# Optimization experiments

Measured on AMD Instinct MI355X. Metric: run time of the kernel, lower is better.

## Reference

```python
import jax, jax.numpy as jnp
import numpy as np
import math

C, H, L, V = 1024, 16, 2, 32000
D = C // H  # head_dim = 64
FF = 4 * C
B, T = 1, 2048
EPS = 1e-5

def _alibi_slopes(n_heads):
    start = 2 ** (-2 ** (-(math.log2(n_heads) - 3)))
    return np.array([start * start ** i for i in range(n_heads)], dtype=np.float32)

SLOPES = jnp.asarray(_alibi_slopes(H))

def _sym_ln(x, w, b):
    # per-head-channel LayerNorm over head_dim, scalar scale/bias per head
    xh = x.reshape(x.shape[0], x.shape[1], H, D)
    mu = xh.mean(-1, keepdims=True)
    var = ((xh - mu) ** 2).mean(-1, keepdims=True)
    n = (xh - mu) / jnp.sqrt(var + EPS)
    n = n * w[None, None, :, None] + b[None, None, :, None]
    return n.reshape(x.shape)

def _alibi_bias(t):
    pos = jnp.arange(t)[None, :] - jnp.arange(t)[:, None]  # j - i
    pos = jnp.minimum(pos, 0).astype(jnp.float32)
    return SLOPES[:, None, None] * pos[None, :, :]  # (H, T, T)

def _block(x, ln1_w, ln1_b, ln2_w, ln2_b, attn_w, attn_b, v_tmp, proj_tmp, fc_w, fc_b, pw, pb):
    b_, t_, _ = x.shape
    h_in = _sym_ln(x, ln1_w, ln1_b)
    qk = h_in @ attn_w.T + attn_b  # (B, T, 2C)
    q, k = jnp.split(qk, 2, axis=-1)
    # Kronecker/block-diagonal V: per-head (head_dim x head_dim) matmul, x @ M^T per head
    xh = h_in.reshape(b_, t_, H, D)
    v = jnp.einsum('bthd,hed->bthe', xh, v_tmp)  # (B, T, H, D)
    q = q.reshape(b_, t_, H, D).transpose(0, 2, 1, 3)
    k = k.reshape(b_, t_, H, D).transpose(0, 2, 1, 3)
    v = v.transpose(0, 2, 1, 3)
    scale = 1.0 / math.sqrt(D)
    scores = jnp.einsum('bhqd,bhkd->bhqk', q, k) * scale
    scores = scores + _alibi_bias(t_)[None]  # note: no causal mask in original code
    att = jax.nn.softmax(scores, axis=-1)
    y = jnp.einsum('bhqk,bhkd->bhqd', att, v)
    y = y.transpose(0, 2, 1, 3)  # (B, T, H, D)
    y = jnp.einsum('bthd,hed->bthe', y, proj_tmp).reshape(b_, t_, C)
    x = x + y
    h2 = _sym_ln(x, ln2_w, ln2_b)
    f = jax.nn.gelu(h2 @ fc_w.T + fc_b, approximate=False)
    x = x + (f @ pw.T + pb)
    return x

def setup_inputs() -> dict:
    key = jax.random.key(0)
    ks = jax.random.split(key, 12)
    s = 0.02
    return {
        'idx': jax.random.randint(ks[0], (B, T), 0, V, dtype=jnp.int32),
        'wte': jax.random.normal(ks[1], (V, C), jnp.float32) * s,
        'ln1_w': jnp.ones((L, H), jnp.float32),
        'ln1_b': jnp.zeros((L, H), jnp.float32),
        'ln2_w': jnp.ones((L, H), jnp.float32),
        'ln2_b': jnp.zeros((L, H), jnp.float32),
        'lnf_w': jnp.ones((H,), jnp.float32),
        'lnf_b': jnp.zeros((H,), jnp.float32),
        'attn_w': jax.random.normal(ks[2], (L, 2 * C, C), jnp.float32) * s,
        'attn_b': jnp.zeros((L, 2 * C), jnp.float32),
        'v_tmp': jax.random.normal(ks[3], (L, H, D, D), jnp.float32) * s,
        'proj_tmp': jax.random.normal(ks[4], (L, H, D, D), jnp.float32) * s,
        'fc_w': jax.random.normal(ks[5], (L, FF, C), jnp.float32) * s,
        'fc_b': jnp.zeros((L, FF), jnp.float32),
        'proj_w': jax.random.normal(ks[6], (L, C, FF), jnp.float32) * s,
        'proj_b': jnp.zeros((L, C), jnp.float32),
    }

def reference(idx, wte, ln1_w, ln1_b, ln2_w, ln2_b, lnf_w, lnf_b,
              attn_w, attn_b, v_tmp, proj_tmp, fc_w, fc_b, proj_w, proj_b):
    x = wte[idx]  # (B, T, C)
    for l in range(L):
        x = _block(x, ln1_w[l], ln1_b[l], ln2_w[l], ln2_b[l],
                   attn_w[l], attn_b[l], v_tmp[l], proj_tmp[l],
                   fc_w[l], fc_b[l], proj_w[l], proj_b[l])
    x = _sym_ln(x, lnf_w, lnf_b)
    logits = x @ wte.T  # tied lm_head
    return logits
```

## Files before the change

### kernel.cpp

```cpp
#include <hip/hip_runtime.h>
#include <cstdint>
#include <cstddef>

#define T_SEQ 2048
#define C_DIM 1024
#define H_HEADS 16
#define D_HEAD 64
#define FF_DIM 4096
#define V_VOCAB 32000
#define L_LAYERS 2

typedef unsigned short u16;
typedef short bf16x8 __attribute__((ext_vector_type(8)));
typedef float f32x4 __attribute__((ext_vector_type(4)));

__device__ inline u16 f2bf(float f) {
  unsigned u = __float_as_uint(f);
  u += 0x7fffu + ((u >> 16) & 1u);
  return (u16)(u >> 16);
}
__device__ inline float bf2f(u16 h) { return __uint_as_float(((unsigned)h) << 16); }

#define OFF_WTEBF   0ULL
#define OFF_ATTNBF  65536000ULL
#define OFF_FCBF    73924608ULL
#define OFF_PRJBF   90701824ULL
#define OFF_X       107479040ULL
#define OFF_HBF     115867648ULL
#define OFF_QKBF    120061952ULL
#define OFF_VT      128450560ULL
#define OFF_Y       132644864ULL
#define OFF_FBF     141033472ULL
#define OFF_VWBF    157810688ULL
#define OFF_PWBF    158072832ULL
#define ARENA_BYTES 158334976ULL

__device__ __align__(1024) unsigned char g_arena[ARENA_BYTES];

__global__ void cvt_bf16_k(const float4* __restrict__ in, ushort4* __restrict__ out, int n4) {
  int i = blockIdx.x * 256 + threadIdx.x;
  if (i < n4) {
    float4 v = in[i];
    out[i] = make_ushort4(f2bf(v.x), f2bf(v.y), f2bf(v.z), f2bf(v.w));
  }
}

__global__ void cvt_multi_k(const float4* __restrict__ s0, const float4* __restrict__ s1,
                            const float4* __restrict__ s2, const float4* __restrict__ s3,
                            const float4* __restrict__ s4,
                            ushort4* __restrict__ d0, ushort4* __restrict__ d1,
                            ushort4* __restrict__ d2, ushort4* __restrict__ d3,
                            ushort4* __restrict__ d4) {
  int g = blockIdx.x * 256 + threadIdx.x;
  const float4* s; ushort4* d; int off;
  if (g < 1048576)      { s = s0; d = d0; off = g; }
  else if (g < 3145728) { s = s1; d = d1; off = g - 1048576; }
  else if (g < 5242880) { s = s2; d = d2; off = g - 3145728; }
  else if (g < 5275648) { s = s3; d = d3; off = g - 5242880; }
  else                  { s = s4; d = d4; off = g - 5275648; }
  float4 v = s[off];
  d[off] = make_ushort4(f2bf(v.x), f2bf(v.y), f2bf(v.z), f2bf(v.w));
}

__global__ void embed_k(const int* __restrict__ idx, const float4* __restrict__ wte,
                        float4* __restrict__ x) {
  int t = blockIdx.x;
  int r = idx[t];
  x[(size_t)t * 256 + threadIdx.x] = wte[(size_t)r * 256 + threadIdx.x];
}

__global__ void symln_k(const float* __restrict__ x, const float* __restrict__ w,
                        const float* __restrict__ b, u16* __restrict__ out) {
  int t = blockIdx.x;
  int wv = threadIdx.x >> 6, lane = threadIdx.x & 63;
  #pragma unroll
  for (int hh = 0; hh < 4; hh++) {
    int h = wv * 4 + hh;
    float v = x[(size_t)t * C_DIM + h * 64 + lane];
    float s = v, s2 = v * v;
    #pragma unroll
    for (int m = 32; m; m >>= 1) { s += __shfl_xor(s, m); s2 += __shfl_xor(s2, m); }
    float mu = s * (1.f / 64.f);
    float var = s2 * (1.f / 64.f) - mu * mu;
    float n = (v - mu) * rsqrtf(var + 1e-5f) * w[h] + b[h];
    out[(size_t)t * C_DIM + h * 64 + lane] = f2bf(n);
  }
}

template <int NROWS, int ROWBYTES, int WAVES>
__device__ inline void stage_rows(u16* lds, const u16* __restrict__ g, int ld,
                                  int wid, int lane) {
  constexpr int PASSES = (NROWS * ROWBYTES) / (WAVES * 1024);
  #pragma unroll
  for (int i = 0; i < PASSES; i++) {
    int base = (i * WAVES + wid) * 1024;
    int o = base + lane * 16;
    int u = o ^ (((o / ROWBYTES) & 7) << 4);
    int row = u / ROWBYTES, colb = u % ROWBYTES;
    const u16* src = g + (size_t)row * ld + (colb >> 1);
    __builtin_amdgcn_global_load_lds((const __attribute__((address_space(1))) void*)src,
                                     (__attribute__((address_space(3))) void*)(lds + base / 2),
                                     16, 0, 0);
  }
}

__device__ inline void stage_pass(u16* lds, const u16* __restrict__ g, int ld,
                                  int i, int wid, int lane) {
  int base = (i * 8 + wid) * 1024;
  int o = base + lane * 16;
  int u = o ^ (((o >> 7) & 7) << 4);
  int row = u >> 7, colb = u & 127;
  const u16* src = g + (size_t)row * ld + (colb >> 1);
  __builtin_amdgcn_global_load_lds((const __attribute__((address_space(1))) void*)src,
                                   (__attribute__((address_space(3))) void*)(lds + base / 2),
                                   16, 0, 0);
}

__global__ __launch_bounds__(256) void flash_k(const u16* __restrict__ qk,
                                               const u16* __restrict__ vt,
                                               u16* __restrict__ y) {
  int h = blockIdx.y;
  int q0 = blockIdx.x * 64;
  int tid = threadIdx.x, wid = tid >> 6, lane = tid & 63;
  int g4 = lane >> 4, l15 = lane & 15;
  __shared__ u16 Kl[128 * 64];
  __shared__ u16 Vl[64 * 128];
  __shared__ u16 Pl[64 * 128];
  float slope = exp2f(-0.5f * (float)(h + 1));

  bf16x8 qf[2];
  const u16* qb = qk + (size_t)(q0 + wid * 16) * 2048 + h * 64;
  #pragma unroll
  for (int kk = 0; kk < 2; kk++)
    qf[kk] = *(const bf16x8*)(qb + (size_t)l15 * 2048 + kk * 32 + g4 * 8);

  f32x4 lsum = (f32x4){0.f, 0.f, 0.f, 0.f};
  f32x4 oacc[4];
  #pragma unroll
  for (int n = 0; n < 4; n++) oacc[n] = (f32x4){0.f, 0.f, 0.f, 0.f};

  const u16* kbase = qk + 1024 + h * 64;
  const u16* vbase = vt + (size_t)h * 64 * T_SEQ;

  for (int kt = 0; kt < T_SEQ / 128; kt++) {
    int k0 = kt * 128;
    stage_rows<128, 128, 4>(Kl, kbase + (size_t)k0 * 2048, 2048, wid, lane);
    stage_rows<64, 256, 4>(Vl, vbase + k0, T_SEQ, wid, lane);
    __syncthreads();

    f32x4 s[8];
    #pragma unroll
    for (int n = 0; n < 8; n++) s[n] = (f32x4){0.f, 0.f, 0.f, 0.f};
    #pragma unroll
    for (int kk = 0; kk < 2; kk++) {
      #pragma unroll
      for (int n = 0; n < 8; n++) {
        int r = n * 16 + l15;
        int b = (r * 128 + kk * 64 + g4 * 16) ^ ((r & 7) << 4);
        bf16x8 kf = *(const bf16x8*)((const char*)Kl + b);
        s[n] = __builtin_amdgcn_mfma_f32_16x16x32_bf16(qf[kk], kf, s[n], 0, 0, 0);
      }
    }

    int iq = q0 + wid * 16 + g4 * 4;
    #pragma unroll
    for (int n = 0; n < 8; n++) {
      int j = k0 + n * 16 + l15;
      #pragma unroll
      for (int i = 0; i < 4; i++) {
        float v = s[n][i] * 0.125f + slope * fminf((float)(j - (iq + i)), 0.f);
        float p = __expf(v - 8.f);
        lsum[i] += p;
        int pr = wid * 16 + g4 * 4 + i;
        int b = (pr * 256 + (n * 16 + l15) * 2) ^ ((pr & 7) << 4);
        *(u16*)((char*)Pl + b) = f2bf(p);
      }
    }

    #pragma unroll
    for (int kk = 0; kk < 4; kk++) {
      int pr = wid * 16 + l15;
      int pb = (pr * 256 + kk * 64 + g4 * 16) ^ ((pr & 7) << 4);
      bf16x8 pa = *(const bf16x8*)((const char*)Pl + pb);
      #pragma unroll
      for (int n = 0; n < 4; n++) {
        int d = n * 16 + l15;
        int vb = (d * 256 + kk * 64 + g4 * 16) ^ ((d & 7) << 4);
        bf16x8 vf = *(const bf16x8*)((const char*)Vl + vb);
        oacc[n] = __builtin_amdgcn_mfma_f32_16x16x32_bf16(pa, vf, oacc[n], 0, 0, 0);
      }
    }
    __syncthreads();
  }

  #pragma unroll
  for (int i = 0; i < 4; i++) {
    float v = lsum[i];
    #pragma unroll
    for (int msk = 1; msk <= 8; msk <<= 1) v += __shfl_xor(v, msk);
    lsum[i] = v;
  }
  u16* yb = y + (size_t)(q0 + wid * 16) * C_DIM + h * 64;
  #pragma unroll
  for (int n = 0; n < 4; n++)
    #pragma unroll
    for (int i = 0; i < 4; i++)
      yb[(size_t)(g4 * 4 + i) * C_DIM + n * 16 + l15] = f2bf(oacc[n][i] / lsum[i]);
}

#define ASM_VMCNT0 asm volatile("s_waitcnt vmcnt(0)" ::: "memory")

__global__ __launch_bounds__(512, 1) void gemm256_k(const u16* __restrict__ A, int lda,
                                                    const u16* __restrict__ B, int ldb,
                                                    float* __restrict__ C, int ldc,
                                                    int K, int MT) {
  extern __shared__ u16 sm[];
  u16* lsA = sm;
  u16* lsB = sm + 32768;
  int tid = threadIdx.x, wid = tid >> 6, lane = tid & 63;
  int g4 = lane >> 4, l15 = lane & 15;
  int wm = wid >> 2, wn = wid & 3;
  int nwg = gridDim.x, lin = blockIdx.x;
  int chunk = nwg >> 3;
  int w = (lin & 7) * chunk + (lin >> 3);
  int by = w % MT, bx = w / MT;
  const u16* Ab = A + (size_t)(by * 256) * lda;
  const u16* Bb = B + (size_t)(bx * 256) * ldb;

  f32x4 acc[8][4];
  #pragma unroll
  for (int m = 0; m < 8; m++)
    #pragma unroll
    for (int n = 0; n < 4; n++) acc[m][n] = (f32x4){0.f, 0.f, 0.f, 0.f};

  int NT = K >> 6;
  stage_rows<256, 128, 8>(lsA, Ab, lda, wid, lane);
  stage_rows<256, 128, 8>(lsB, Bb, ldb, wid, lane);

  for (int t = 0; t < NT; ++t) {
    int cur = t & 1;
    const char* cA = (const char*)(lsA + cur * 16384);
    const char* cB = (const char*)(lsB + cur * 16384);
    u16* nAl = lsA + (cur ^ 1) * 16384;
    u16* nBl = lsB + (cur ^ 1) * 16384;
    const u16* gA = Ab + (t + 1) * 64;
    const u16* gB = Bb + (t + 1) * 64;
    bool pf = (t + 1 < NT);

    ASM_VMCNT0;
    __builtin_amdgcn_s_barrier();
    __builtin_amdgcn_sched_barrier(0);

    bf16x8 bfr[4], af[4];
    #pragma unroll
    for (int ph = 0; ph < 4; ++ph) {
      const int kk = ph >> 1, mh = ph & 1;
      if (mh == 0) {
        #pragma unroll
        for (int n = 0; n < 4; n++) {
          int r = wn * 64 + n * 16 + l15;
          bfr[n] = *(const bf16x8*)(cB + ((r * 128 + kk * 64 + g4 * 16) ^ ((r & 7) << 4)));
        }
      }
      #pragma unroll
      for (int m = 0; m < 4; m++) {
        int r = wm * 128 + mh * 64 + m * 16 + l15;
        af[m] = *(const bf16x8*)(cA + ((r * 128 + kk * 64 + g4 * 16) ^ ((r & 7) << 4)));
      }
      if (pf) {
        if (ph == 0) { stage_pass(nAl, gA, lda, 0, wid, lane);
                       stage_pass(nAl, gA, lda, 1, wid, lane);
                       stage_pass(nBl, gB, ldb, 0, wid, lane); }
        else if (ph == 1) { stage_pass(nAl, gA, lda, 2, wid, lane);
                            stage_pass(nAl, gA, lda, 3, wid, lane);
                            stage_pass(nBl, gB, ldb, 1, wid, lane); }
        else if (ph == 2) { stage_pass(nBl, gB, ldb, 2, wid, lane);
                            stage_pass(nBl, gB, ldb, 3, wid, lane); }
      }
      __builtin_amdgcn_s_setprio(1);
      #pragma unroll
      for (int m = 0; m < 4; m++)
        #pragma unroll
        for (int n = 0; n < 4; n++)
          acc[mh * 4 + m][n] =
              __builtin_amdgcn_mfma_f32_16x16x32_bf16(af[m], bfr[n], acc[mh * 4 + m][n], 0, 0, 0);
      __builtin_amdgcn_s_setprio(0);
      __builtin_amdgcn_s_barrier();
    }
  }

  int gr0 = by * 256 + wm * 128, gc0 = bx * 256 + wn * 64;
  #pragma unroll
  for (int m = 0; m < 8; m++)
    #pragma unroll
    for (int n = 0; n < 4; n++)
      #pragma unroll
      for (int i = 0; i < 4; i++)
        C[(size_t)(gr0 + m * 16 + g4 * 4 + i) * ldc + gc0 + n * 16 + l15] = acc[m][n][i];
}

template <int BM, int BN, int WM, int WN, int EPI, int MT, int GRID>
__global__ void gemm_nt(const u16* __restrict__ A, int lda, long long sA,
                        const u16* __restrict__ B, int ldb, long long sB,
                        void* __restrict__ C, int ldc, long long sC,
                        int K, const float* __restrict__ bias,
                        const float* __restrict__ resid, int ldr) {
  constexpr int RM = BM / WM, RN = BN / WN;
  constexpr int MR = RM / 16, NR = RN / 16;
  __shared__ u16 lsA[BM * 64];
  __shared__ u16 lsB[BN * 64];
  int tid = threadIdx.x, wid = tid >> 6, lane = tid & 63;
  int wm = wid / WN, wn = wid % WN;
  int lin, z;
  if constexpr (GRID == 1) {
    lin = blockIdx.x; z = blockIdx.y;
  } else {
    int nwg = gridDim.x, l0 = blockIdx.x;
    int chunk = nwg >> 3;
    lin = (l0 & 7) * chunk + (l0 >> 3);
    z = 0;
  }
  int by = lin % MT, bx = lin / MT;
  int row0 = by * BM, col0 = bx * BN;
  const u16* Ab = A + (size_t)z * sA + (size_t)row0 * lda;
  const u16* Bb = B + (size_t)z * sB + (size_t)col0 * ldb;
  size_t cz = (size_t)z * sC;

  f32x4 acc[MR][NR];
  #pragma unroll
  for (int m = 0; m < MR; m++)
    #pragma unroll
    for (int n = 0; n < NR; n++) acc[m][n] = (f32x4){0.f, 0.f, 0.f, 0.f};

  for (int k0 = 0; k0 < K; k0 += 64) {
    stage_rows<BM, 128, 4>(lsA, Ab + k0, lda, wid, lane);
    stage_rows<BN, 128, 4>(lsB, Bb + k0, ldb, wid, lane);
    __syncthreads();
    #pragma unroll
    for (int kk = 0; kk < 2; kk++) {
      bf16x8 af[MR], bfr[NR];
      #pragma unroll
      for (int m = 0; m < MR; m++) {
        int r = wm * RM + m * 16 + (lane & 15);
        int bofs = (r * 128 + kk * 64 + ((lane >> 4) * 16)) ^ ((r & 7) << 4);
        af[m] = *(const bf16x8*)((const char*)lsA + bofs);
      }
      #pragma unroll
      for (int n = 0; n < NR; n++) {
        int r = wn * RN + n * 16 + (lane & 15);
        int bofs = (r * 128 + kk * 64 + ((lane >> 4) * 16)) ^ ((r & 7) << 4);
        bfr[n] = *(const bf16x8*)((const char*)lsB + bofs);
      }
      #pragma unroll
      for (int m = 0; m < MR; m++)
        #pragma unroll
        for (int n = 0; n < NR; n++)
          acc[m][n] = __builtin_amdgcn_mfma_f32_16x16x32_bf16(af[m], bfr[n], acc[m][n], 0, 0, 0);
    }
    __syncthreads();
  }

  int rbase = row0 + wm * RM, cbase = col0 + wn * RN;
  #pragma unroll
  for (int m = 0; m < MR; m++)
    #pragma unroll
    for (int n = 0; n < NR; n++)
      #pragma unroll
      for (int i = 0; i < 4; i++) {
        int gr = rbase + m * 16 + ((lane >> 4) * 4) + i;
        int gc = cbase + n * 16 + (lane & 15);
        size_t idx = cz + (size_t)gr * ldc + gc;
        float v = acc[m][n][i];
        if constexpr (EPI == 0) {
          ((float*)C)[idx] = v;
        } else if constexpr (EPI == 1) {
          v += bias[gc];
          ((u16*)C)[idx] = f2bf(v);
        } else if constexpr (EPI == 2) {
          ((u16*)C)[idx] = f2bf(v);
        } else if constexpr (EPI == 3) {
          v += bias[gc];
          v = 0.5f * v * (1.f + erff(v * 0.70710678118654752f));
          ((u16*)C)[idx] = f2bf(v);
        } else if constexpr (EPI == 4) {
          v += bias[gc] + resid[(size_t)gr * ldr + gc];
          ((float*)C)[idx] = v;
        } else {
          ((float*)C)[idx] += v;
        }
      }
}

extern "C" void kernel_launch(void* const* d_in, const int* in_sizes, int n_in,
                              void* d_out, int out_size, void* d_ws, size_t ws_size,
                              hipStream_t stream) {
  (void)in_sizes; (void)n_in; (void)out_size; (void)d_ws; (void)ws_size;
  const int*   idx    = (const int*)d_in[0];
  const float* wte    = (const float*)d_in[1];
  const float* ln1w   = (const float*)d_in[2];
  const float* ln1b   = (const float*)d_in[3];
  const float* ln2w   = (const float*)d_in[4];
  const float* ln2b   = (const float*)d_in[5];
  const float* lnfw   = (const float*)d_in[6];
  const float* lnfb   = (const float*)d_in[7];
  const float* attw   = (const float*)d_in[8];
  const float* attb   = (const float*)d_in[9];
  const float* vtmp   = (const float*)d_in[10];
  const float* ptmp   = (const float*)d_in[11];
  const float* fcw    = (const float*)d_in[12];
  const float* fcb    = (const float*)d_in[13];
  const float* prjw   = (const float*)d_in[14];
  const float* prjb   = (const float*)d_in[15];
  float* out = (float*)d_out;

  unsigned char* ar = nullptr;
  hipGetSymbolAddress((void**)&ar, HIP_SYMBOL(g_arena));
  u16*   wtebf  = (u16*)(ar + OFF_WTEBF);
  u16*   attnbf = (u16*)(ar + OFF_ATTNBF);
  u16*   fcbf   = (u16*)(ar + OFF_FCBF);
  u16*   prjbf  = (u16*)(ar + OFF_PRJBF);
  float* x      = (float*)(ar + OFF_X);
  u16*   hbf    = (u16*)(ar + OFF_HBF);
  u16*   qkbf   = (u16*)(ar + OFF_QKBF);
  u16*   vt     = (u16*)(ar + OFF_VT);
  u16*   ybf    = (u16*)(ar + OFF_Y);
  u16*   fbf    = (u16*)(ar + OFF_FBF);
  u16*   vwbf   = (u16*)(ar + OFF_VWBF);
  u16*   pwbf   = (u16*)(ar + OFF_PWBF);

  hipFuncSetAttribute((const void*)gemm256_k,
                      hipFuncAttributeMaxDynamicSharedMemorySize, 131072);

  cvt_bf16_k<<<dim3((V_VOCAB * C_DIM / 4) / 256), 256, 0, stream>>>(
      (const float4*)wte, (ushort4*)wtebf, V_VOCAB * C_DIM / 4);
  cvt_multi_k<<<dim3(20736), 256, 0, stream>>>(
      (const float4*)attw, (const float4*)fcw, (const float4*)prjw,
      (const float4*)vtmp, (const float4*)ptmp,
      (ushort4*)attnbf, (ushort4*)fcbf, (ushort4*)prjbf,
      (ushort4*)vwbf, (ushort4*)pwbf);

  embed_k<<<dim3(T_SEQ), 256, 0, stream>>>(idx, (const float4*)wte, (float4*)x);

  for (int l = 0; l < L_LAYERS; l++) {
    symln_k<<<dim3(T_SEQ), 256, 0, stream>>>(x, ln1w + l * H_HEADS, ln1b + l * H_HEADS, hbf);
    gemm_nt<64, 128, 2, 2, 1, 32, 0><<<dim3((2 * C_DIM / 128) * (T_SEQ / 64)), 256, 0, stream>>>(
        hbf, C_DIM, 0, attnbf + (size_t)l * 2 * C_DIM * C_DIM, C_DIM, 0,
        qkbf, 2 * C_DIM, 0, C_DIM, attb + l * 2 * C_DIM, nullptr, 0);
    gemm_nt<64, 128, 2, 2, 2, 1, 1><<<dim3(T_SEQ / 128, H_HEADS), 256, 0, stream>>>(
        vwbf + (size_t)l * H_HEADS * 4096, 64, 4096, hbf, C_DIM, 64,
        vt, T_SEQ, (long long)64 * T_SEQ, 64, nullptr, nullptr, 0);
    flash_k<<<dim3(T_SEQ / 64, H_HEADS), 256, 0, stream>>>(qkbf, vt, ybf);
    gemm_nt<128, 64, 4, 1, 5, 16, 1><<<dim3(T_SEQ / 128, H_HEADS), 256, 0, stream>>>(
        ybf, C_DIM, 64, pwbf + (size_t)l * H_HEADS * 4096, 64, 4096,
        x, C_DIM, 64, 64, nullptr, nullptr, 0);
    symln_k<<<dim3(T_SEQ), 256, 0, stream>>>(x, ln2w + l * H_HEADS, ln2b + l * H_HEADS, hbf);
    gemm_nt<128, 128, 2, 2, 3, 16, 0><<<dim3((FF_DIM / 128) * (T_SEQ / 128)), 256, 0, stream>>>(
        hbf, C_DIM, 0, fcbf + (size_t)l * FF_DIM * C_DIM, C_DIM, 0,
        fbf, FF_DIM, 0, C_DIM, fcb + l * FF_DIM, nullptr, 0);
    gemm_nt<64, 128, 2, 2, 4, 32, 0><<<dim3((C_DIM / 128) * (T_SEQ / 64)), 256, 0, stream>>>(
        fbf, FF_DIM, 0, prjbf + (size_t)l * C_DIM * FF_DIM, FF_DIM, 0,
        x, C_DIM, 0, FF_DIM, prjb + l * C_DIM, x, C_DIM);
  }
  symln_k<<<dim3(T_SEQ), 256, 0, stream>>>(x, lnfw, lnfb, hbf);
  gemm256_k<<<dim3((V_VOCAB / 256) * (T_SEQ / 256)), 512, 131072, stream>>>(
      hbf, C_DIM, wtebf, C_DIM, out, V_VOCAB, C_DIM, T_SEQ / 256);
}
```

Before: 600.6 us.

## Double-buffer K tiles in LDS and load V straight into registers

The flash attention kernel now keeps two LDS buffers for K and prefetches the next 128-key tile while the current one is being used. V is no longer staged through LDS: each wave loads its V fragments directly from global memory into registers. This removes the trailing per-iteration __syncthreads and some of the LDS traffic, so K loads for the next tile overlap with compute. The cost is that every wave reads the full V tile, which multiplies global/L2 reads of V, and the V fragments take extra VGPRs, which may lower occupancy.

Measured after the change: 739.3 us. 1.23x slower.

```diff
diff --git a/kernel.cpp b/kernel.cpp
--- a/kernel.cpp
+++ b/kernel.cpp
@@ -123,8 +123,7 @@
   int q0 = blockIdx.x * 64;
   int tid = threadIdx.x, wid = tid >> 6, lane = tid & 63;
   int g4 = lane >> 4, l15 = lane & 15;
-  __shared__ u16 Kl[128 * 64];
-  __shared__ u16 Vl[64 * 128];
+  __shared__ u16 Kl[2][128 * 64];
   __shared__ u16 Pl[64 * 128];
   float slope = exp2f(-0.5f * (float)(h + 1));
 
@@ -142,11 +141,27 @@
   const u16* kbase = qk + 1024 + h * 64;
   const u16* vbase = vt + (size_t)h * 64 * T_SEQ;
 
+  stage_rows<128, 128, 4>(Kl[0], kbase, 2048, wid, lane);
+
   for (int kt = 0; kt < T_SEQ / 128; kt++) {
     int k0 = kt * 128;
-    stage_rows<128, 128, 4>(Kl, kbase + (size_t)k0 * 2048, 2048, wid, lane);
-    stage_rows<64, 256, 4>(Vl, vbase + k0, T_SEQ, wid, lane);
-    __syncthreads();
+    const char* cK = (const char*)Kl[kt & 1];
+    asm volatile("s_waitcnt vmcnt(0)" ::: "memory");
+    __builtin_amdgcn_s_barrier();
+    __builtin_amdgcn_sched_barrier(0);
+
+    bf16x8 vf[4][4];
+    #pragma unroll
+    for (int kk = 0; kk < 4; kk++)
+      #pragma unroll
+      for (int n = 0; n < 4; n++)
+        vf[kk][n] = *(const bf16x8*)(vbase + (size_t)(n * 16 + l15) * T_SEQ +
+                                     k0 + kk * 32 + g4 * 8);
+    __builtin_amdgcn_sched_barrier(0);
+
+    if (kt + 1 < T_SEQ / 128)
+      stage_rows<128, 128, 4>(Kl[(kt + 1) & 1], kbase + (size_t)(k0 + 128) * 2048,
+                              2048, wid, lane);
 
     f32x4 s[8];
     #pragma unroll
@@ -157,7 +172,7 @@
       for (int n = 0; n < 8; n++) {
         int r = n * 16 + l15;
         int b = (r * 128 + kk * 64 + g4 * 16) ^ ((r & 7) << 4);
-        bf16x8 kf = *(const bf16x8*)((const char*)Kl + b);
+        bf16x8 kf = *(const bf16x8*)(cK + b);
         s[n] = __builtin_amdgcn_mfma_f32_16x16x32_bf16(qf[kk], kf, s[n], 0, 0, 0);
       }
     }
@@ -183,14 +198,9 @@
       int pb = (pr * 256 + kk * 64 + g4 * 16) ^ ((pr & 7) << 4);
       bf16x8 pa = *(const bf16x8*)((const char*)Pl + pb);
       #pragma unroll
-      for (int n = 0; n < 4; n++) {
-        int d = n * 16 + l15;
-        int vb = (d * 256 + kk * 64 + g4 * 16) ^ ((d & 7) << 4);
-        bf16x8 vf = *(const bf16x8*)((const char*)Vl + vb);
-        oacc[n] = __builtin_amdgcn_mfma_f32_16x16x32_bf16(pa, vf, oacc[n], 0, 0, 0);
-      }
+      for (int n = 0; n < 4; n++)
+        oacc[n] = __builtin_amdgcn_mfma_f32_16x16x32_bf16(pa, vf[kk][n], oacc[n], 0, 0, 0);
     }
-    __syncthreads();
   }
 
   #pragma unroll
```

## Split flash attention across key dimension with separate combine kernel

Applied to the files above, without the earlier changes.

Flash attention now splits the key range into four chunks along a new grid z dimension. Each block writes unnormalized fp32 partial outputs and row sums to a scratch arena. A new combine kernel sums the partials, normalizes them and writes the bf16 output. This raises block count and occupancy for attention, at the cost of extra global traffic and one more launch per layer.

Measured after the change: 619.7 us. 3.2% more time.

```diff
diff --git a/kernel.cpp b/kernel.cpp
--- a/kernel.cpp
+++ b/kernel.cpp
@@ -9,6 +9,7 @@
 #define FF_DIM 4096
 #define V_VOCAB 32000
 #define L_LAYERS 2
+#define NSPLIT 4
 
 typedef unsigned short u16;
 typedef short bf16x8 __attribute__((ext_vector_type(8)));
@@ -33,7 +34,9 @@
 #define OFF_FBF     141033472ULL
 #define OFF_VWBF    157810688ULL
 #define OFF_PWBF    158072832ULL
-#define ARENA_BYTES 158334976ULL
+#define OFF_OPART   158334976ULL
+#define OFF_LPART   191889408ULL
+#define ARENA_BYTES 192413696ULL
 
 __device__ __align__(1024) unsigned char g_arena[ARENA_BYTES];
 
@@ -118,9 +121,11 @@
 
 __global__ __launch_bounds__(256) void flash_k(const u16* __restrict__ qk,
                                                const u16* __restrict__ vt,
-                                               u16* __restrict__ y) {
+                                               float* __restrict__ opart,
+                                               float* __restrict__ lpart) {
   int h = blockIdx.y;
   int q0 = blockIdx.x * 64;
+  int zs = blockIdx.z;
   int tid = threadIdx.x, wid = tid >> 6, lane = tid & 63;
   int g4 = lane >> 4, l15 = lane & 15;
   __shared__ u16 Kl[128 * 64];
@@ -142,7 +147,7 @@
   const u16* kbase = qk + 1024 + h * 64;
   const u16* vbase = vt + (size_t)h * 64 * T_SEQ;
 
-  for (int kt = 0; kt < T_SEQ / 128; kt++) {
+  for (int kt = zs * 4; kt < zs * 4 + 4; kt++) {
     int k0 = kt * 128;
     stage_rows<128, 128, 4>(Kl, kbase + (size_t)k0 * 2048, 2048, wid, lane);
     stage_rows<64, 256, 4>(Vl, vbase + k0, T_SEQ, wid, lane);
@@ -200,12 +205,35 @@
     for (int msk = 1; msk <= 8; msk <<= 1) v += __shfl_xor(v, msk);
     lsum[i] = v;
   }
-  u16* yb = y + (size_t)(q0 + wid * 16) * C_DIM + h * 64;
+  float* ob = opart + ((size_t)zs * T_SEQ + q0 + wid * 16) * C_DIM + h * 64;
   #pragma unroll
   for (int n = 0; n < 4; n++)
     #pragma unroll
     for (int i = 0; i < 4; i++)
-      yb[(size_t)(g4 * 4 + i) * C_DIM + n * 16 + l15] = f2bf(oacc[n][i] / lsum[i]);
+      ob[(size_t)(g4 * 4 + i) * C_DIM + n * 16 + l15] = oacc[n][i];
+  if (l15 == 0) {
+    #pragma unroll
+    for (int i = 0; i < 4; i++)
+      lpart[((size_t)zs * H_HEADS + h) * T_SEQ + q0 + wid * 16 + g4 * 4 + i] = lsum[i];
+  }
+}
+
+__global__ void fcomb_k(const float* __restrict__ opart, const float* __restrict__ lpart,
+                        u16* __restrict__ y) {
+  int t = blockIdx.x;
+  int c = threadIdx.x * 4;
+  int h = c >> 6;
+  float4 s = make_float4(0.f, 0.f, 0.f, 0.f);
+  float l = 0.f;
+  #pragma unroll
+  for (int z = 0; z < NSPLIT; z++) {
+    float4 o = *(const float4*)(opart + ((size_t)z * T_SEQ + t) * C_DIM + c);
+    s.x += o.x; s.y += o.y; s.z += o.z; s.w += o.w;
+    l += lpart[((size_t)z * H_HEADS + h) * T_SEQ + t];
+  }
+  float inv = 1.f / l;
+  *(ushort4*)(y + (size_t)t * C_DIM + c) =
+      make_ushort4(f2bf(s.x * inv), f2bf(s.y * inv), f2bf(s.z * inv), f2bf(s.w * inv));
 }
 
 #define ASM_VMCNT0 asm volatile("s_waitcnt vmcnt(0)" ::: "memory")
@@ -427,6 +455,8 @@
   u16*   fbf    = (u16*)(ar + OFF_FBF);
   u16*   vwbf   = (u16*)(ar + OFF_VWBF);
   u16*   pwbf   = (u16*)(ar + OFF_PWBF);
+  float* opart  = (float*)(ar + OFF_OPART);
+  float* lpart  = (float*)(ar + OFF_LPART);
 
   hipFuncSetAttribute((const void*)gemm256_k,
                       hipFuncAttributeMaxDynamicSharedMemorySize, 131072);
@@ -449,7 +479,8 @@
     gemm_nt<64, 128, 2, 2, 2, 1, 1><<<dim3(T_SEQ / 128, H_HEADS), 256, 0, stream>>>(
         vwbf + (size_t)l * H_HEADS * 4096, 64, 4096, hbf, C_DIM, 64,
         vt, T_SEQ, (long long)64 * T_SEQ, 64, nullptr, nullptr, 0);
-    flash_k<<<dim3(T_SEQ / 64, H_HEADS), 256, 0, stream>>>(qkbf, vt, ybf);
+    flash_k<<<dim3(T_SEQ / 64, H_HEADS, NSPLIT), 256, 0, stream>>>(qkbf, vt, opart, lpart);
+    fcomb_k<<<dim3(T_SEQ), 256, 0, stream>>>(opart, lpart, ybf);
     gemm_nt<128, 64, 4, 1, 5, 16, 1><<<dim3(T_SEQ / 128, H_HEADS), 256, 0, stream>>>(
         ybf, C_DIM, 64, pwbf + (size_t)l * H_HEADS * 4096, 64, 4096,
         x, C_DIM, 64, 64, nullptr, nullptr, 0);
```

## Transpose QK^T MFMA in flash kernel, pack P stores, retile FC GEMM

Applied to the files above, without the earlier changes.

The flash attention kernel swaps the MFMA operands so each lane holds scores for a single query row across four consecutive keys. That lets the softmax write probabilities as packed bf16x4 stores via v_cvt_pk_bf16_f32 instead of scalar u16 stores, and keeps one scalar row sum that needs only two cross-lane shuffles. The final normalisation multiplies by a reciprocal instead of dividing. Separately, the FC GEMM tile changes from 128x128 to 64x128, doubling the grid, which trades per-block reuse for more parallelism.

Result: faster. 560.2 us (-6.7%).

```diff
diff --git a/kernel.cpp b/kernel.cpp
--- a/kernel.cpp
+++ b/kernel.cpp
@@ -134,13 +134,14 @@
   for (int kk = 0; kk < 2; kk++)
     qf[kk] = *(const bf16x8*)(qb + (size_t)l15 * 2048 + kk * 32 + g4 * 8);
 
-  f32x4 lsum = (f32x4){0.f, 0.f, 0.f, 0.f};
+  float lsum = 0.f;
   f32x4 oacc[4];
   #pragma unroll
   for (int n = 0; n < 4; n++) oacc[n] = (f32x4){0.f, 0.f, 0.f, 0.f};
 
   const u16* kbase = qk + 1024 + h * 64;
   const u16* vbase = vt + (size_t)h * 64 * T_SEQ;
+  int myq = q0 + wid * 16 + l15;
 
   for (int kt = 0; kt < T_SEQ / 128; kt++) {
     int k0 = kt * 128;
@@ -158,28 +159,31 @@
         int r = n * 16 + l15;
         int b = (r * 128 + kk * 64 + g4 * 16) ^ ((r & 7) << 4);
         bf16x8 kf = *(const bf16x8*)((const char*)Kl + b);
-        s[n] = __builtin_amdgcn_mfma_f32_16x16x32_bf16(qf[kk], kf, s[n], 0, 0, 0);
+        s[n] = __builtin_amdgcn_mfma_f32_16x16x32_bf16(kf, qf[kk], s[n], 0, 0, 0);
       }
     }
 
-    int iq = q0 + wid * 16 + g4 * 4;
+    float fd = (float)(k0 + g4 * 4 - myq);
+    int pr = wid * 16 + l15;
     #pragma unroll
     for (int n = 0; n < 8; n++) {
-      int j = k0 + n * 16 + l15;
+      float p[4];
       #pragma unroll
       for (int i = 0; i < 4; i++) {
-        float v = s[n][i] * 0.125f + slope * fminf((float)(j - (iq + i)), 0.f);
-        float p = __expf(v - 8.f);
-        lsum[i] += p;
-        int pr = wid * 16 + g4 * 4 + i;
-        int b = (pr * 256 + (n * 16 + l15) * 2) ^ ((pr & 7) << 4);
-        *(u16*)((char*)Pl + b) = f2bf(p);
-      }
+        float dj = fd + (float)(n * 16 + i);
+        float a2 = fmaf(slope, fminf(dj, 0.f), -8.f);
+        p[i] = __expf(fmaf(s[n][i], 0.125f, a2));
+        lsum += p[i];
+      }
+      unsigned lo, hi;
+      asm("v_cvt_pk_bf16_f32 %0, %1, %2" : "=v"(lo) : "v"(p[0]), "v"(p[1]));
+      asm("v_cvt_pk_bf16_f32 %0, %1, %2" : "=v"(hi) : "v"(p[2]), "v"(p[3]));
+      int b = (pr * 256 + n * 32 + g4 * 8) ^ ((pr & 7) << 4);
+      *(uint2*)((char*)Pl + b) = make_uint2(lo, hi);
     }
 
     #pragma unroll
     for (int kk = 0; kk < 4; kk++) {
-      int pr = wid * 16 + l15;
       int pb = (pr * 256 + kk * 64 + g4 * 16) ^ ((pr & 7) << 4);
       bf16x8 pa = *(const bf16x8*)((const char*)Pl + pb);
       #pragma unroll
@@ -193,19 +197,18 @@
     __syncthreads();
   }
 
-  #pragma unroll
-  for (int i = 0; i < 4; i++) {
-    float v = lsum[i];
-    #pragma unroll
-    for (int msk = 1; msk <= 8; msk <<= 1) v += __shfl_xor(v, msk);
-    lsum[i] = v;
-  }
+  lsum += __shfl_xor(lsum, 16);
+  lsum += __shfl_xor(lsum, 32);
+  float linv[4];
+  #pragma unroll
+  for (int i = 0; i < 4; i++) linv[i] = 1.f / __shfl(lsum, g4 * 4 + i);
+
   u16* yb = y + (size_t)(q0 + wid * 16) * C_DIM + h * 64;
   #pragma unroll
   for (int n = 0; n < 4; n++)
     #pragma unroll
     for (int i = 0; i < 4; i++)
-      yb[(size_t)(g4 * 4 + i) * C_DIM + n * 16 + l15] = f2bf(oacc[n][i] / lsum[i]);
+      yb[(size_t)(g4 * 4 + i) * C_DIM + n * 16 + l15] = f2bf(oacc[n][i] * linv[i]);
 }
 
 #define ASM_VMCNT0 asm volatile("s_waitcnt vmcnt(0)" ::: "memory")
@@ -454,7 +457,7 @@
         ybf, C_DIM, 64, pwbf + (size_t)l * H_HEADS * 4096, 64, 4096,
         x, C_DIM, 64, 64, nullptr, nullptr, 0);
     symln_k<<<dim3(T_SEQ), 256, 0, stream>>>(x, ln2w + l * H_HEADS, ln2b + l * H_HEADS, hbf);
-    gemm_nt<128, 128, 2, 2, 3, 16, 0><<<dim3((FF_DIM / 128) * (T_SEQ / 128)), 256, 0, stream>>>(
+    gemm_nt<64, 128, 2, 2, 3, 32, 0><<<dim3((FF_DIM / 128) * (T_SEQ / 64)), 256, 0, stream>>>(
         hbf, C_DIM, 0, fcbf + (size_t)l * FF_DIM * C_DIM, C_DIM, 0,
         fbf, FF_DIM, 0, C_DIM, fcb + l * FF_DIM, nullptr, 0);
     gemm_nt<64, 128, 2, 2, 4, 32, 0><<<dim3((C_DIM / 128) * (T_SEQ / 64)), 256, 0, stream>>>(
```
